# Kernel optimization log

Measured on AMD Instinct MI355X. Metric: run time of the kernel, lower is better.

## Reference

```python
import jax, jax.numpy as jnp
import numpy as np

N_NODES = 50000
N_EDGES = 800000
D_IN = 128
D_OUT = 128
ALPHA = 0.2  # LeakyReLU negative slope


def setup_inputs() -> dict:
    key = jax.random.key(0)
    k1, k2, k3, k4 = jax.random.split(key, 4)
    x = jax.random.normal(k1, (N_NODES, D_IN), dtype=jnp.float32)
    W = jax.random.normal(k2, (D_IN, D_OUT), dtype=jnp.float32) * (1.414 / np.sqrt(D_IN))
    a = jax.random.normal(k3, (2 * D_OUT, 1), dtype=jnp.float32) * 0.1
    edge_index = jax.random.randint(k4, (2, N_EDGES), 0, N_NODES, dtype=jnp.int64)
    return {"x": x, "W": W, "a": a, "edge_index": edge_index}


def reference(x, W, a, edge_index):
    # h: (N, D_OUT)
    h = x @ W
    src, dst = edge_index[0], edge_index[1]
    # e_i = leakyrelu([h[src]; h[dst]] @ a) == leakyrelu((h@a1)[src] + (h@a2)[dst])
    a1 = a[:D_OUT, 0]
    a2 = a[D_OUT:, 0]
    s1 = h @ a1  # (N,)
    s2 = h @ a2  # (N,)
    e = jax.nn.leaky_relu(s1[src] + s2[dst], negative_slope=ALPHA)  # (E,)
    # Global softmax over all edges (faithful to F.softmax(edge_e, dim=0))
    attention = jax.nn.softmax(e)  # (E,)
    # output[dst] += attention * h[src]  (scatter-add)
    msgs = attention[:, None] * h[src]  # (E, D_OUT)
    output = jax.ops.segment_sum(msgs, dst, num_segments=N_NODES)
    return output
```

## Files before the change

kernel.cpp:

```cpp
#include <hip/hip_runtime.h>
#include <hip/hip_bf16.h>

#define N_NODES 50000
#define N_EDGES 800000
#define D 128
#define ALPHA 0.2f
#define NEG_INF -1e30f

#define KB_BLOCKS 3125
#define LDS_STRIDE 272

#define SCAN_PER 52
#define SCAN_PAD (1024 * SCAN_PER)

typedef __attribute__((ext_vector_type(8))) short short8;
typedef __attribute__((ext_vector_type(4))) float floatx4;

__device__ __forceinline__ unsigned int f2bf(float v)
{
    __hip_bfloat16 b = __float2bfloat16(v);
    return (unsigned int)*reinterpret_cast<unsigned short*>(&b);
}
__device__ __forceinline__ float bf_lo(unsigned int u)
{
    return __uint_as_float(u << 16);
}
__device__ __forceinline__ float bf_hi(unsigned int u)
{
    return __uint_as_float(u & 0xFFFF0000u);
}

__global__ __launch_bounds__(1024) void k_prep(
    const float* __restrict__ W, const float* __restrict__ a,
    float* __restrict__ w12, unsigned short* __restrict__ wb,
    int* __restrict__ deg)
{
    const int t = threadIdx.x;
    const int b = blockIdx.x;
    deg[b * 1024 + t] = 0;

    if (b < 4) {
        const int g = b * 64 + (t >> 4);
        const int c = t & 15;
        const int which = g >> 7;
        const int r = g & 127;
        const float* wp = W + (size_t)r * D + c * 8;
        const float* ap = a + which * D + c * 8;
        const float4 u0 = *(const float4*)(wp);
        const float4 u1 = *(const float4*)(wp + 4);
        const float4 c0 = *(const float4*)(ap);
        const float4 c1 = *(const float4*)(ap + 4);
        float p = u0.x * c0.x + u0.y * c0.y + u0.z * c0.z + u0.w * c0.w
                + u1.x * c1.x + u1.y * c1.y + u1.z * c1.z + u1.w * c1.w;
        #pragma unroll
        for (int mask = 8; mask >= 1; mask >>= 1)
            p += __shfl_xor(p, mask);
        if (c == 0) w12[which * D + r] = p;
    } else if (b < 20) {
        const int f = (b - 4) * 1024 + t;
        const int j    = f & 7;
        const int lane = (f >> 3) & 63;
        const int half = (f >> 9) & 1;
        const int kt   = (f >> 10) & 3;
        const int wv   = f >> 12;
        const int q    = lane >> 4;
        const int nIdx = lane & 15;
        const float val =
            W[(size_t)(kt * 32 + q * 8 + j) * D + wv * 32 + 2 * nIdx + half];
        wb[f] = (unsigned short)f2bf(val);
    }
}

__global__ __launch_bounds__(256) void k_sc(
    const float* __restrict__ x, const float* __restrict__ w12,
    float* __restrict__ s1, float* __restrict__ s2)
{
    const int t = threadIdx.x;
    const int r = t >> 4;
    const int c = t & 15;
    const int row = blockIdx.x * 16 + r;
    const float* xp = x + (size_t)row * D + c * 8;
    const float4 v0 = *(const float4*)(xp);
    const float4 v1 = *(const float4*)(xp + 4);
    const float* w1 = w12 + c * 8;
    const float* w2 = w12 + D + c * 8;
    float p1 = v0.x * w1[0] + v0.y * w1[1] + v0.z * w1[2] + v0.w * w1[3]
             + v1.x * w1[4] + v1.y * w1[5] + v1.z * w1[6] + v1.w * w1[7];
    float p2 = v0.x * w2[0] + v0.y * w2[1] + v0.z * w2[2] + v0.w * w2[3]
             + v1.x * w2[4] + v1.y * w2[5] + v1.z * w2[6] + v1.w * w2[7];
    #pragma unroll
    for (int mask = 8; mask >= 1; mask >>= 1) {
        p1 += __shfl_xor(p1, mask);
        p2 += __shfl_xor(p2, mask);
    }
    if (c == 0) { s1[row] = p1; s2[row] = p2; }
}

__global__ __launch_bounds__(256) void k_fused(
    const float* __restrict__ x, const unsigned short* __restrict__ wb,
    const int* __restrict__ ei, const float* __restrict__ s1,
    const float* __restrict__ s2, unsigned short* __restrict__ hb,
    int* __restrict__ deg, int* __restrict__ rank, float* __restrict__ ve,
    float* __restrict__ bm, float* __restrict__ bs)
{
    __shared__ unsigned char lds[16 * LDS_STRIDE];
    __shared__ float red[8];
    const int t = threadIdx.x;
    const int rowbase = blockIdx.x * 16;

    const int e = blockIdx.x * 256 + t;
    const int sN = ei[e];
    const int dN = ei[N_EDGES + e];
    const float s1g = s1[sN];
    const float s2g = s2[dN];

    const int r = t >> 4;
    const int c = t & 15;
    const float* xp = x + (size_t)(rowbase + r) * D + c * 8;
    const float4 v0 = *(const float4*)(xp);
    const float4 v1 = *(const float4*)(xp + 4);

    const int lane = t & 63;
    const int wv = t >> 6;
    const int q = lane >> 4;
    const int nIdx = lane & 15;
    const int n0 = wv * 32;
    const short8* wbp = (const short8*)wb;
    short8 B[2][4];
    #pragma unroll
    for (int kt = 0; kt < 4; ++kt) {
        B[0][kt] = wbp[((wv * 4 + kt) * 2 + 0) * 64 + lane];
        B[1][kt] = wbp[((wv * 4 + kt) * 2 + 1) * 64 + lane];
    }

    {
        uint4 pk;
        pk.x = f2bf(v0.x) | (f2bf(v0.y) << 16);
        pk.y = f2bf(v0.z) | (f2bf(v0.w) << 16);
        pk.z = f2bf(v1.x) | (f2bf(v1.y) << 16);
        pk.w = f2bf(v1.z) | (f2bf(v1.w) << 16);
        *(uint4*)(lds + r * LDS_STRIDE + c * 16) = pk;
    }
    __syncthreads();

    const unsigned char* ab = lds + nIdx * LDS_STRIDE + q * 16;
    const short8 A0 = *(const short8*)(ab);
    const short8 A1 = *(const short8*)(ab + 64);
    const short8 A2 = *(const short8*)(ab + 128);
    const short8 A3 = *(const short8*)(ab + 192);

    floatx4 acc0 = {0.f, 0.f, 0.f, 0.f};
    floatx4 acc1 = {0.f, 0.f, 0.f, 0.f};
    acc0 = __builtin_amdgcn_mfma_f32_16x16x32_bf16(A0, B[0][0], acc0, 0, 0, 0);
    acc1 = __builtin_amdgcn_mfma_f32_16x16x32_bf16(A0, B[1][0], acc1, 0, 0, 0);
    acc0 = __builtin_amdgcn_mfma_f32_16x16x32_bf16(A1, B[0][1], acc0, 0, 0, 0);
    acc1 = __builtin_amdgcn_mfma_f32_16x16x32_bf16(A1, B[1][1], acc1, 0, 0, 0);
    acc0 = __builtin_amdgcn_mfma_f32_16x16x32_bf16(A2, B[0][2], acc0, 0, 0, 0);
    acc1 = __builtin_amdgcn_mfma_f32_16x16x32_bf16(A2, B[1][2], acc1, 0, 0, 0);
    acc0 = __builtin_amdgcn_mfma_f32_16x16x32_bf16(A3, B[0][3], acc0, 0, 0, 0);
    acc1 = __builtin_amdgcn_mfma_f32_16x16x32_bf16(A3, B[1][3], acc1, 0, 0, 0);

    #pragma unroll
    for (int i = 0; i < 4; ++i) {
        const int row = rowbase + q * 4 + i;
        const unsigned int pk = f2bf(acc0[i]) | (f2bf(acc1[i]) << 16);
        *(unsigned int*)(hb + (size_t)row * D + n0 + 2 * nIdx) = pk;
    }

    rank[e] = atomicAdd(&deg[dN], 1);
    float v = s1g + s2g;
    v = v > 0.f ? v : ALPHA * v;
    ve[e] = v;

    float m = v;
    #pragma unroll
    for (int mask = 32; mask >= 1; mask >>= 1)
        m = fmaxf(m, __shfl_xor(m, mask));
    if (lane == 0) red[wv] = m;
    __syncthreads();
    m = fmaxf(fmaxf(red[0], red[1]), fmaxf(red[2], red[3]));
    float sx = __expf(v - m);
    #pragma unroll
    for (int mask = 32; mask >= 1; mask >>= 1)
        sx += __shfl_xor(sx, mask);
    if (lane == 0) red[4 + wv] = sx;
    __syncthreads();
    if (t == 0) {
        bm[blockIdx.x] = m;
        bs[blockIdx.x] = red[4] + red[5] + red[6] + red[7];
    }
}

__global__ __launch_bounds__(1024) void k_mid(
    const int* __restrict__ deg, int* __restrict__ offs,
    const float* __restrict__ bm, const float* __restrict__ bs,
    float* __restrict__ MZ)
{
    const int t = threadIdx.x;
    const int lane = t & 63;
    const int wv = t >> 6;

    if (blockIdx.x == 0) {
        __shared__ int wsum[16];
        const int base = t * SCAN_PER;
        int4 v[13];
        const int4* dp = (const int4*)(deg + base);
        int s = 0;
        #pragma unroll
        for (int k = 0; k < 13; ++k) {
            v[k] = dp[k];
            s += v[k].x + v[k].y + v[k].z + v[k].w;
        }
        int inc = s;
        #pragma unroll
        for (int off = 1; off < 64; off <<= 1) {
            int u = __shfl_up(inc, off);
            if (lane >= off) inc += u;
        }
        if (lane == 63) wsum[wv] = inc;
        __syncthreads();
        if (wv == 0 && lane < 16) {
            int wval = wsum[lane];
            int winc = wval;
            #pragma unroll
            for (int off = 1; off < 16; off <<= 1) {
                int u = __shfl_up(winc, off);
                if (lane >= off) winc += u;
            }
            wsum[lane] = winc - wval;
        }
        __syncthreads();
        int run = wsum[wv] + (inc - s);
        int4* op = (int4*)(offs + base);
        #pragma unroll
        for (int k = 0; k < 13; ++k) {
            int4 o;
            o.x = run;             run += v[k].x;
            o.y = run;             run += v[k].y;
            o.z = run;             run += v[k].z;
            o.w = run;             run += v[k].w;
            op[k] = o;
        }
        return;
    }

    __shared__ float red[16];
    float m = NEG_INF;
    for (int i = t; i < KB_BLOCKS; i += 1024)
        m = fmaxf(m, bm[i]);
    #pragma unroll
    for (int mask = 32; mask >= 1; mask >>= 1)
        m = fmaxf(m, __shfl_xor(m, mask));
    if (lane == 0) red[wv] = m;
    __syncthreads();
    float M = red[0];
    #pragma unroll
    for (int w = 1; w < 16; ++w) M = fmaxf(M, red[w]);
    __syncthreads();
    float sx = 0.f;
    for (int i = t; i < KB_BLOCKS; i += 1024)
        sx += bs[i] * __expf(bm[i] - M);
    #pragma unroll
    for (int mask = 32; mask >= 1; mask >>= 1)
        sx += __shfl_xor(sx, mask);
    if (lane == 0) red[wv] = sx;
    __syncthreads();
    if (t == 0) {
        float Z = 0.f;
        #pragma unroll
        for (int w = 0; w < 16; ++w) Z += red[w];
        MZ[0] = M;
        MZ[1] = Z;
    }
}

__global__ __launch_bounds__(256) void k_post(
    const int* __restrict__ ei, const int* __restrict__ offs,
    const int* __restrict__ rank, const float* __restrict__ ve,
    uint2* __restrict__ csr64)
{
    const int e = blockIdx.x * 256 + threadIdx.x;
    const int sN = ei[e];
    const int dN = ei[N_EDGES + e];
    uint2 rec;
    rec.x = (unsigned int)sN;
    rec.y = __float_as_uint(ve[e]);
    csr64[offs[dN] + rank[e]] = rec;
}

__global__ __launch_bounds__(256) void k_gather(
    const uint2* __restrict__ csr64, const int* __restrict__ offs,
    const unsigned short* __restrict__ hb, const float* __restrict__ MZ,
    float* __restrict__ out)
{
    const int node = (blockIdx.x * blockDim.x + threadIdx.x) >> 6;
    if (node >= N_NODES) return;
    const int lane = threadIdx.x & 63;
    const float M = MZ[0];
    const float invZ = 1.0f / MZ[1];
    const int beg = offs[node];
    const int end = offs[node + 1];

    float a0 = 0.f, a1 = 0.f, b0 = 0.f, b1 = 0.f;
    float c0 = 0.f, c1 = 0.f, d0 = 0.f, d1 = 0.f;
    float e0 = 0.f, e1 = 0.f, f0 = 0.f, f1 = 0.f;
    float g0 = 0.f, g1 = 0.f, h0 = 0.f, h1 = 0.f;

    for (int cb = beg; cb < end; cb += 64) {
        const int n = min(64, end - cb);
        uint2 rec;
        if (cb + lane < end) {
            rec = csr64[cb + lane];
        } else {
            rec.x = 0u;
            rec.y = 0xFF800000u;
        }
        const int srcl = (int)rec.x;
        const float attl = __expf(__uint_as_float(rec.y) - M) * invZ;

        int j = 0;
        for (; j + 7 < n; j += 8) {
            const int i0 = __shfl(srcl, j);
            const int i1 = __shfl(srcl, j + 1);
            const int i2 = __shfl(srcl, j + 2);
            const int i3 = __shfl(srcl, j + 3);
            const int i4 = __shfl(srcl, j + 4);
            const int i5 = __shfl(srcl, j + 5);
            const int i6 = __shfl(srcl, j + 6);
            const int i7 = __shfl(srcl, j + 7);
            const float w0 = __shfl(attl, j);
            const float w1 = __shfl(attl, j + 1);
            const float w2 = __shfl(attl, j + 2);
            const float w3 = __shfl(attl, j + 3);
            const float w4 = __shfl(attl, j + 4);
            const float w5 = __shfl(attl, j + 5);
            const float w6 = __shfl(attl, j + 6);
            const float w7 = __shfl(attl, j + 7);
            const unsigned int u0 = *(const unsigned int*)(hb + (size_t)i0 * D + lane * 2);
            const unsigned int u1 = *(const unsigned int*)(hb + (size_t)i1 * D + lane * 2);
            const unsigned int u2 = *(const unsigned int*)(hb + (size_t)i2 * D + lane * 2);
            const unsigned int u3 = *(const unsigned int*)(hb + (size_t)i3 * D + lane * 2);
            const unsigned int u4 = *(const unsigned int*)(hb + (size_t)i4 * D + lane * 2);
            const unsigned int u5 = *(const unsigned int*)(hb + (size_t)i5 * D + lane * 2);
            const unsigned int u6 = *(const unsigned int*)(hb + (size_t)i6 * D + lane * 2);
            const unsigned int u7 = *(const unsigned int*)(hb + (size_t)i7 * D + lane * 2);
            a0 += w0 * bf_lo(u0); a1 += w0 * bf_hi(u0);
            b0 += w1 * bf_lo(u1); b1 += w1 * bf_hi(u1);
            c0 += w2 * bf_lo(u2); c1 += w2 * bf_hi(u2);
            d0 += w3 * bf_lo(u3); d1 += w3 * bf_hi(u3);
            e0 += w4 * bf_lo(u4); e1 += w4 * bf_hi(u4);
            f0 += w5 * bf_lo(u5); f1 += w5 * bf_hi(u5);
            g0 += w6 * bf_lo(u6); g1 += w6 * bf_hi(u6);
            h0 += w7 * bf_lo(u7); h1 += w7 * bf_hi(u7);
        }
        for (; j + 3 < n; j += 4) {
            const int i0 = __shfl(srcl, j);
            const int i1 = __shfl(srcl, j + 1);
            const int i2 = __shfl(srcl, j + 2);
            const int i3 = __shfl(srcl, j + 3);
            const float w0 = __shfl(attl, j);
            const float w1 = __shfl(attl, j + 1);
            const float w2 = __shfl(attl, j + 2);
            const float w3 = __shfl(attl, j + 3);
            const unsigned int u0 = *(const unsigned int*)(hb + (size_t)i0 * D + lane * 2);
            const unsigned int u1 = *(const unsigned int*)(hb + (size_t)i1 * D + lane * 2);
            const unsigned int u2 = *(const unsigned int*)(hb + (size_t)i2 * D + lane * 2);
            const unsigned int u3 = *(const unsigned int*)(hb + (size_t)i3 * D + lane * 2);
            a0 += w0 * bf_lo(u0); a1 += w0 * bf_hi(u0);
            b0 += w1 * bf_lo(u1); b1 += w1 * bf_hi(u1);
            c0 += w2 * bf_lo(u2); c1 += w2 * bf_hi(u2);
            d0 += w3 * bf_lo(u3); d1 += w3 * bf_hi(u3);
        }
        for (; j < n; ++j) {
            const int i0 = __shfl(srcl, j);
            const float w0 = __shfl(attl, j);
            const unsigned int u0 = *(const unsigned int*)(hb + (size_t)i0 * D + lane * 2);
            a0 += w0 * bf_lo(u0); a1 += w0 * bf_hi(u0);
        }
    }
    float2 r;
    r.x = ((a0 + b0) + (c0 + d0)) + ((e0 + f0) + (g0 + h0));
    r.y = ((a1 + b1) + (c1 + d1)) + ((e1 + f1) + (g1 + h1));
    *(float2*)(out + (size_t)node * D + lane * 2) = r;
}

extern "C" void kernel_launch(void* const* d_in, const int* in_sizes, int n_in,
                              void* d_out, int out_size, void* d_ws, size_t ws_size,
                              hipStream_t stream)
{
    const float* x = (const float*)d_in[0];
    const float* W = (const float*)d_in[1];
    const float* a = (const float*)d_in[2];
    const int* ei = (const int*)d_in[3];
    float* out = (float*)d_out;

    char* wsb = (char*)d_ws;
    uint2* csr64 = (uint2*)wsb;
    unsigned short* hb = (unsigned short*)(wsb + (size_t)N_EDGES * 8);
    unsigned short* wb = hb + (size_t)N_NODES * D;
    int* rank     = (int*)(wb + 16384);
    float* ve     = (float*)(rank + N_EDGES);
    float* s1     = ve + N_EDGES;
    float* s2     = s1 + N_NODES;
    int*   deg    = (int*)(s2 + N_NODES);
    int*   offs   = deg + SCAN_PAD;
    float* w12    = (float*)(offs + SCAN_PAD);
    float* bm     = w12 + 2 * D;
    float* bs     = bm + KB_BLOCKS;
    float* MZ     = bs + KB_BLOCKS;

    k_prep<<<SCAN_PAD / 1024, 1024, 0, stream>>>(W, a, w12, wb, deg);
    k_sc<<<N_NODES / 16, 256, 0, stream>>>(x, w12, s1, s2);
    k_fused<<<N_NODES / 16, 256, 0, stream>>>(x, wb, ei, s1, s2, hb,
                                              deg, rank, ve, bm, bs);
    k_mid<<<2, 1024, 0, stream>>>(deg, offs, bm, bs, MZ);
    k_post<<<KB_BLOCKS, 256, 0, stream>>>(ei, offs, rank, ve, csr64);
    k_gather<<<(N_NODES * 64 + 255) / 256, 256, 0, stream>>>(
        csr64, offs, hb, MZ, out);
}
```

Measured before the change: 177.7 us.

## Fuse score computation into GEMM kernel and drop max-subtracted softmax pass

Folds the per-node attention score computation into the MFMA kernel so x is read once, and moves the edge score, exp and normalizer accumulation into the CSR scatter kernel with a global atomic sum. The global max reduction and the intermediate edge-value buffer are removed, and the gather uses precomputed exponentials. This trades numerical safety (no max subtraction, risk of overflow for large scores) for fewer kernels and less memory traffic.

Result: slower. 205.5 us (+15.6%).

```diff
diff --git a/kernel.cpp b/kernel.cpp
--- a/kernel.cpp
+++ b/kernel.cpp
@@ -5,7 +5,6 @@
 #define N_EDGES 800000
 #define D 128
 #define ALPHA 0.2f
-#define NEG_INF -1e30f
 
 #define KB_BLOCKS 3125
 #define LDS_STRIDE 272
@@ -33,11 +32,12 @@
 __global__ __launch_bounds__(1024) void k_prep(
     const float* __restrict__ W, const float* __restrict__ a,
     float* __restrict__ w12, unsigned short* __restrict__ wb,
-    int* __restrict__ deg)
+    int* __restrict__ deg, float* __restrict__ Z)
 {
     const int t = threadIdx.x;
     const int b = blockIdx.x;
     deg[b * 1024 + t] = 0;
+    if (b == 20 && t == 0) Z[0] = 0.f;
 
     if (b < 4) {
         const int g = b * 64 + (t >> 4);
@@ -71,48 +71,15 @@
     }
 }
 
-__global__ __launch_bounds__(256) void k_sc(
+__global__ __launch_bounds__(256) void k_fused(
     const float* __restrict__ x, const float* __restrict__ w12,
-    float* __restrict__ s1, float* __restrict__ s2)
-{
-    const int t = threadIdx.x;
-    const int r = t >> 4;
-    const int c = t & 15;
-    const int row = blockIdx.x * 16 + r;
-    const float* xp = x + (size_t)row * D + c * 8;
-    const float4 v0 = *(const float4*)(xp);
-    const float4 v1 = *(const float4*)(xp + 4);
-    const float* w1 = w12 + c * 8;
-    const float* w2 = w12 + D + c * 8;
-    float p1 = v0.x * w1[0] + v0.y * w1[1] + v0.z * w1[2] + v0.w * w1[3]
-             + v1.x * w1[4] + v1.y * w1[5] + v1.z * w1[6] + v1.w * w1[7];
-    float p2 = v0.x * w2[0] + v0.y * w2[1] + v0.z * w2[2] + v0.w * w2[3]
-             + v1.x * w2[4] + v1.y * w2[5] + v1.z * w2[6] + v1.w * w2[7];
-    #pragma unroll
-    for (int mask = 8; mask >= 1; mask >>= 1) {
-        p1 += __shfl_xor(p1, mask);
-        p2 += __shfl_xor(p2, mask);
-    }
-    if (c == 0) { s1[row] = p1; s2[row] = p2; }
-}
-
-__global__ __launch_bounds__(256) void k_fused(
-    const float* __restrict__ x, const unsigned short* __restrict__ wb,
-    const int* __restrict__ ei, const float* __restrict__ s1,
-    const float* __restrict__ s2, unsigned short* __restrict__ hb,
-    int* __restrict__ deg, int* __restrict__ rank, float* __restrict__ ve,
-    float* __restrict__ bm, float* __restrict__ bs)
+    const unsigned short* __restrict__ wb, const int* __restrict__ ei,
+    unsigned short* __restrict__ hb, float* __restrict__ s1,
+    float* __restrict__ s2, int* __restrict__ deg, int* __restrict__ rank)
 {
     __shared__ unsigned char lds[16 * LDS_STRIDE];
-    __shared__ float red[8];
     const int t = threadIdx.x;
     const int rowbase = blockIdx.x * 16;
-
-    const int e = blockIdx.x * 256 + t;
-    const int sN = ei[e];
-    const int dN = ei[N_EDGES + e];
-    const float s1g = s1[sN];
-    const float s2g = s2[dN];
 
     const int r = t >> 4;
     const int c = t & 15;
@@ -134,6 +101,19 @@
     }
 
     {
+        const float* w1 = w12 + c * 8;
+        const float* w2 = w12 + D + c * 8;
+        float p1 = v0.x * w1[0] + v0.y * w1[1] + v0.z * w1[2] + v0.w * w1[3]
+                 + v1.x * w1[4] + v1.y * w1[5] + v1.z * w1[6] + v1.w * w1[7];
+        float p2 = v0.x * w2[0] + v0.y * w2[1] + v0.z * w2[2] + v0.w * w2[3]
+                 + v1.x * w2[4] + v1.y * w2[5] + v1.z * w2[6] + v1.w * w2[7];
+        #pragma unroll
+        for (int mask = 8; mask >= 1; mask >>= 1) {
+            p1 += __shfl_xor(p1, mask);
+            p2 += __shfl_xor(p2, mask);
+        }
+        if (c == 0) { s1[rowbase + r] = p1; s2[rowbase + r] = p2; }
+
         uint4 pk;
         pk.x = f2bf(v0.x) | (f2bf(v0.y) << 16);
         pk.y = f2bf(v0.z) | (f2bf(v0.w) << 16);
@@ -167,137 +147,100 @@
         *(unsigned int*)(hb + (size_t)row * D + n0 + 2 * nIdx) = pk;
     }
 
-    rank[e] = atomicAdd(&deg[dN], 1);
-    float v = s1g + s2g;
-    v = v > 0.f ? v : ALPHA * v;
-    ve[e] = v;
-
-    float m = v;
-    #pragma unroll
-    for (int mask = 32; mask >= 1; mask >>= 1)
-        m = fmaxf(m, __shfl_xor(m, mask));
-    if (lane == 0) red[wv] = m;
-    __syncthreads();
-    m = fmaxf(fmaxf(red[0], red[1]), fmaxf(red[2], red[3]));
-    float sx = __expf(v - m);
-    #pragma unroll
-    for (int mask = 32; mask >= 1; mask >>= 1)
-        sx += __shfl_xor(sx, mask);
-    if (lane == 0) red[4 + wv] = sx;
-    __syncthreads();
-    if (t == 0) {
-        bm[blockIdx.x] = m;
-        bs[blockIdx.x] = red[4] + red[5] + red[6] + red[7];
-    }
-}
-
-__global__ __launch_bounds__(1024) void k_mid(
-    const int* __restrict__ deg, int* __restrict__ offs,
-    const float* __restrict__ bm, const float* __restrict__ bs,
-    float* __restrict__ MZ)
+    const int e = blockIdx.x * 256 + t;
+    rank[e] = atomicAdd(&deg[ei[N_EDGES + e]], 1);
+}
+
+__global__ __launch_bounds__(1024) void k_scan(
+    const int* __restrict__ deg, int* __restrict__ offs)
 {
     const int t = threadIdx.x;
     const int lane = t & 63;
     const int wv = t >> 6;
-
-    if (blockIdx.x == 0) {
-        __shared__ int wsum[16];
-        const int base = t * SCAN_PER;
-        int4 v[13];
-        const int4* dp = (const int4*)(deg + base);
-        int s = 0;
+    __shared__ int wsum[16];
+    const int base = t * SCAN_PER;
+    int4 v[13];
+    const int4* dp = (const int4*)(deg + base);
+    int s = 0;
+    #pragma unroll
+    for (int k = 0; k < 13; ++k) {
+        v[k] = dp[k];
+        s += v[k].x + v[k].y + v[k].z + v[k].w;
+    }
+    int inc = s;
+    #pragma unroll
+    for (int off = 1; off < 64; off <<= 1) {
+        int u = __shfl_up(inc, off);
+        if (lane >= off) inc += u;
+    }
+    if (lane == 63) wsum[wv] = inc;
+    __syncthreads();
+    if (wv == 0 && lane < 16) {
+        int wval = wsum[lane];
+        int winc = wval;
         #pragma unroll
-        for (int k = 0; k < 13; ++k) {
-            v[k] = dp[k];
-            s += v[k].x + v[k].y + v[k].z + v[k].w;
-        }
-        int inc = s;
-        #pragma unroll
-        for (int off = 1; off < 64; off <<= 1) {
-            int u = __shfl_up(inc, off);
-            if (lane >= off) inc += u;
-        }
-        if (lane == 63) wsum[wv] = inc;
-        __syncthreads();
-        if (wv == 0 && lane < 16) {
-            int wval = wsum[lane];
-            int winc = wval;
-            #pragma unroll
-            for (int off = 1; off < 16; off <<= 1) {
-                int u = __shfl_up(winc, off);
-                if (lane >= off) winc += u;
-            }
-            wsum[lane] = winc - wval;
-        }
-        __syncthreads();
-        int run = wsum[wv] + (inc - s);
-        int4* op = (int4*)(offs + base);
-        #pragma unroll
-        for (int k = 0; k < 13; ++k) {
-            int4 o;
-            o.x = run;             run += v[k].x;
-            o.y = run;             run += v[k].y;
-            o.z = run;             run += v[k].z;
-            o.w = run;             run += v[k].w;
-            op[k] = o;
-        }
-        return;
-    }
-
-    __shared__ float red[16];
-    float m = NEG_INF;
-    for (int i = t; i < KB_BLOCKS; i += 1024)
-        m = fmaxf(m, bm[i]);
-    #pragma unroll
-    for (int mask = 32; mask >= 1; mask >>= 1)
-        m = fmaxf(m, __shfl_xor(m, mask));
-    if (lane == 0) red[wv] = m;
+        for (int off = 1; off < 16; off <<= 1) {
+            int u = __shfl_up(winc, off);
+            if (lane >= off) winc += u;
+        }
+        wsum[lane] = winc - wval;
+    }
     __syncthreads();
-    float M = red[0];
-    #pragma unroll
-    for (int w = 1; w < 16; ++w) M = fmaxf(M, red[w]);
-    __syncthreads();
-    float sx = 0.f;
-    for (int i = t; i < KB_BLOCKS; i += 1024)
-        sx += bs[i] * __expf(bm[i] - M);
+    int run = wsum[wv] + (inc - s);
+    int4* op = (int4*)(offs + base);
+    #pragma unroll
+    for (int k = 0; k < 13; ++k) {
+        int4 o;
+        o.x = run;             run += v[k].x;
+        o.y = run;             run += v[k].y;
+        o.z = run;             run += v[k].z;
+        o.w = run;             run += v[k].w;
+        op[k] = o;
+    }
+}
+
+__global__ __launch_bounds__(256) void k_post(
+    const int* __restrict__ ei, const float* __restrict__ s1,
+    const float* __restrict__ s2, const int* __restrict__ offs,
+    const int* __restrict__ rank, uint2* __restrict__ csr64,
+    float* __restrict__ Z)
+{
+    __shared__ float red[4];
+    const int t = threadIdx.x;
+    const int lane = t & 63;
+    const int wv = t >> 6;
+    const int e = blockIdx.x * 256 + t;
+    const int sN = ei[e];
+    const int dN = ei[N_EDGES + e];
+    const int rk = rank[e];
+    const int off = offs[dN];
+    float v = s1[sN] + s2[dN];
+    v = v > 0.f ? v : ALPHA * v;
+    const float ex = __expf(v);
+    uint2 rec;
+    rec.x = (unsigned int)sN;
+    rec.y = __float_as_uint(ex);
+    csr64[off + rk] = rec;
+
+    float sx = ex;
     #pragma unroll
     for (int mask = 32; mask >= 1; mask >>= 1)
         sx += __shfl_xor(sx, mask);
     if (lane == 0) red[wv] = sx;
     __syncthreads();
-    if (t == 0) {
-        float Z = 0.f;
-        #pragma unroll
-        for (int w = 0; w < 16; ++w) Z += red[w];
-        MZ[0] = M;
-        MZ[1] = Z;
-    }
-}
-
-__global__ __launch_bounds__(256) void k_post(
-    const int* __restrict__ ei, const int* __restrict__ offs,
-    const int* __restrict__ rank, const float* __restrict__ ve,
-    uint2* __restrict__ csr64)
-{
-    const int e = blockIdx.x * 256 + threadIdx.x;
-    const int sN = ei[e];
-    const int dN = ei[N_EDGES + e];
-    uint2 rec;
-    rec.x = (unsigned int)sN;
-    rec.y = __float_as_uint(ve[e]);
-    csr64[offs[dN] + rank[e]] = rec;
+    if (t == 0)
+        atomicAdd(Z, (red[0] + red[1]) + (red[2] + red[3]));
 }
 
 __global__ __launch_bounds__(256) void k_gather(
     const uint2* __restrict__ csr64, const int* __restrict__ offs,
-    const unsigned short* __restrict__ hb, const float* __restrict__ MZ,
+    const unsigned short* __restrict__ hb, const float* __restrict__ Z,
     float* __restrict__ out)
 {
     const int node = (blockIdx.x * blockDim.x + threadIdx.x) >> 6;
     if (node >= N_NODES) return;
     const int lane = threadIdx.x & 63;
-    const float M = MZ[0];
-    const float invZ = 1.0f / MZ[1];
+    const float invZ = 1.0f / Z[0];
     const int beg = offs[node];
     const int end = offs[node + 1];
 
@@ -313,10 +256,10 @@
             rec = csr64[cb + lane];
         } else {
             rec.x = 0u;
-            rec.y = 0xFF800000u;
+            rec.y = 0u;
         }
         const int srcl = (int)rec.x;
-        const float attl = __expf(__uint_as_float(rec.y) - M) * invZ;
+        const float attl = __uint_as_float(rec.y) * invZ;
 
         int j = 0;
         for (; j + 7 < n; j += 8) {
@@ -399,22 +342,18 @@
     unsigned short* hb = (unsigned short*)(wsb + (size_t)N_EDGES * 8);
     unsigned short* wb = hb + (size_t)N_NODES * D;
     int* rank     = (int*)(wb + 16384);
-    float* ve     = (float*)(rank + N_EDGES);
-    float* s1     = ve + N_EDGES;
+    float* s1     = (float*)(rank + N_EDGES);
     float* s2     = s1 + N_NODES;
     int*   deg    = (int*)(s2 + N_NODES);
     int*   offs   = deg + SCAN_PAD;
     float* w12    = (float*)(offs + SCAN_PAD);
-    float* bm     = w12 + 2 * D;
-    float* bs     = bm + KB_BLOCKS;
-    float* MZ     = bs + KB_BLOCKS;
-
-    k_prep<<<SCAN_PAD / 1024, 1024, 0, stream>>>(W, a, w12, wb, deg);
-    k_sc<<<N_NODES / 16, 256, 0, stream>>>(x, w12, s1, s2);
-    k_fused<<<N_NODES / 16, 256, 0, stream>>>(x, wb, ei, s1, s2, hb,
-                                              deg, rank, ve, bm, bs);
-    k_mid<<<2, 1024, 0, stream>>>(deg, offs, bm, bs, MZ);
-    k_post<<<KB_BLOCKS, 256, 0, stream>>>(ei, offs, rank, ve, csr64);
+    float* Z      = w12 + 2 * D;
+
+    k_prep<<<SCAN_PAD / 1024, 1024, 0, stream>>>(W, a, w12, wb, deg, Z);
+    k_fused<<<N_NODES / 16, 256, 0, stream>>>(x, w12, wb, ei, hb, s1, s2,
+                                              deg, rank);
+    k_scan<<<1, 1024, 0, stream>>>(deg, offs);
+    k_post<<<KB_BLOCKS, 256, 0, stream>>>(ei, s1, s2, offs, rank, csr64, Z);
     k_gather<<<(N_NODES * 64 + 255) / 256, 256, 0, stream>>>(
-        csr64, offs, hb, MZ, out);
-}
+        csr64, offs, hb, Z, out);
+}
```
